# Kernel optimization log

Hardware: AMD Instinct MI355X
Metric: run time of the kernel (lower is better)

Reference implementation:

```python
import jax, jax.numpy as jnp
import numpy as np

N_NODES = 50000
N_EDGES = 1600000
F_IN = 128
C = 64          # block in/out channels
EF = 64         # edge MLP hidden dim
BLOCKS = 3
MLP_DIM = 128
N_CLASSES = 10
N_GRAPHS = 512
EPS = 1e-5


def setup_inputs() -> dict:
    key = jax.random.key(0)
    ks = jax.random.split(key, 32)
    s = 0.05
    inp = {
        "x": jax.random.normal(ks[0], (N_NODES, F_IN), jnp.float32),
        "edge_index": jax.random.randint(ks[1], (2, N_EDGES), 0, N_NODES, jnp.int64),
        "batch": jnp.sort(jax.random.randint(ks[2], (N_NODES,), 0, N_GRAPHS, jnp.int64)),
        "fc0_w": jax.random.normal(ks[3], (F_IN, C), jnp.float32) * s,
        "fc0_b": jnp.zeros((C,), jnp.float32),
        "fc1_w": jax.random.normal(ks[4], (BLOCKS * C, MLP_DIM), jnp.float32) * s,
        "fc1_b": jnp.zeros((MLP_DIM,), jnp.float32),
        "fc2_w": jax.random.normal(ks[5], (MLP_DIM, N_CLASSES), jnp.float32) * s,
        "fc2_b": jnp.zeros((N_CLASSES,), jnp.float32),
    }
    for i in range(BLOCKS):
        k = 6 + 4 * i
        inp[f"bn_g{i}"] = jnp.ones((C,), jnp.float32)
        inp[f"bn_b{i}"] = jnp.zeros((C,), jnp.float32)
        inp[f"w1_{i}"] = jax.random.normal(ks[k], (2 * C, EF), jnp.float32) * s
        inp[f"b1_{i}"] = jnp.zeros((EF,), jnp.float32)
        inp[f"w2_{i}"] = jax.random.normal(ks[k + 1], (EF, C), jnp.float32) * s
        inp[f"b2_{i}"] = jnp.zeros((C,), jnp.float32)
    return inp


def _batchnorm(x, g, b):
    mu = jnp.mean(x, axis=0)
    var = jnp.var(x, axis=0)
    return (x - mu) * jax.lax.rsqrt(var + EPS) * g + b


def _edge_conv(x, src, dst, w1, b1, w2, b2):
    # PyG-style EdgeConv: msg = MLP(concat[x_i, x_j - x_i]), max-aggregate at i
    xi = x[dst]                                  # [E, C]
    xj = x[src]                                  # [E, C]
    h = jax.nn.relu(jnp.concatenate([xi, xj - xi], axis=-1) @ w1 + b1)  # [E, EF]
    m = h @ w2 + b2                              # [E, C]
    agg = jax.ops.segment_max(m, dst, num_segments=N_NODES)
    return jnp.where(jnp.isfinite(agg), agg, 0.0)


def reference(x, edge_index, batch, fc0_w, fc0_b, fc1_w, fc1_b, fc2_w, fc2_b,
              bn_g0, bn_b0, w1_0, b1_0, w2_0, b2_0,
              bn_g1, bn_b1, w1_1, b1_1, w2_1, b2_1,
              bn_g2, bn_b2, w1_2, b1_2, w2_2, b2_2):
    src, dst = edge_index[0], edge_index[1]
    h = x @ fc0_w + fc0_b                        # [N, C]
    blocks = [(bn_g0, bn_b0, w1_0, b1_0, w2_0, b2_0),
              (bn_g1, bn_b1, w1_1, b1_1, w2_1, b2_1),
              (bn_g2, bn_b2, w1_2, b1_2, w2_2, b2_2)]
    xs = []
    for (g, b, w1, b1, w2, b2) in blocks:
        h = _batchnorm(h, g, b)
        h = jax.nn.relu(_edge_conv(h, src, dst, w1, b1, w2, b2))
        xs.append(h)
    cat = jnp.concatenate(xs, axis=-1)           # [N, 3C]
    # global mean pool over graphs
    sums = jax.ops.segment_sum(cat, batch, num_segments=N_GRAPHS)
    cnt = jax.ops.segment_sum(jnp.ones((N_NODES,), cat.dtype), batch,
                              num_segments=N_GRAPHS)
    pooled = sums / jnp.maximum(cnt, 1.0)[:, None]   # [G, 3C]
    hid = jax.nn.relu(pooled @ fc1_w + fc1_b)
    return jax.nn.log_softmax(hid @ fc2_w + fc2_b, axis=-1)
```

## Files before the change

kernel.cpp:

```cpp
#include <hip/hip_runtime.h>
#include <math.h>

#define N_NODES 50000
#define N_TILES 3125
#define N_EDGES 1600000
#define F_IN 128
#define C 64
#define EF 64
#define N_GRAPHS 512
#define MLP_DIM 128
#define N_CLASSES 10
#define EPS 1e-5f
#define NB 196
#define CAPB 16384
#define CHUNK 4096
#define NSLICE 8

typedef __attribute__((ext_vector_type(8))) _Float16 half8;
typedef __attribute__((ext_vector_type(2))) _Float16 half2v;
typedef __attribute__((ext_vector_type(4))) float floatx4;
typedef __attribute__((ext_vector_type(4))) unsigned uintx4;

union Uh { uintx4 v; half2v h[4]; half8 h8; };

__device__ __forceinline__ unsigned short f2h(float a) {
    union { _Float16 f; unsigned short u; } c;
    c.f = (_Float16)a;
    return c.u;
}
__device__ __forceinline__ float h2f(unsigned short u) {
    union { unsigned short u; _Float16 f; } c;
    c.u = u;
    return (float)c.f;
}
__device__ __forceinline__ half2v pk2(float a, float b) {
    auto t = __builtin_amdgcn_cvt_pkrtz(a, b);
    union { decltype(t) i; half2v o; } c;
    c.i = t;
    return c.o;
}

__global__ __launch_bounds__(256) void pass1_kernel(const int* __restrict__ src,
                                                    const int* __restrict__ dst,
                                                    int* __restrict__ gcur,
                                                    unsigned* __restrict__ keys) {
    __shared__ int lcnt[NB], lbase[NB], lcnt2[NB];
    int tid = threadIdx.x;
    int e0 = blockIdx.x * CHUNK;
    unsigned k[CHUNK / 256];
    int bk[CHUNK / 256];
    for (int i = tid; i < NB; i += 256) lcnt[i] = 0;
    __syncthreads();
#pragma unroll
    for (int i = 0; i < CHUNK / 256; i++) {
        int e = e0 + i * 256 + tid;
        if (e < N_EDGES) {
            int d = dst[e];
            k[i] = ((unsigned)d << 16) | (unsigned)src[e];
            bk[i] = d >> 8;
            atomicAdd(&lcnt[bk[i]], 1);
        } else bk[i] = -1;
    }
    __syncthreads();
    for (int i = tid; i < NB; i += 256) {
        int c = lcnt[i];
        lbase[i] = c ? atomicAdd(&gcur[i], c) : 0;
        lcnt2[i] = 0;
    }
    __syncthreads();
#pragma unroll
    for (int i = 0; i < CHUNK / 256; i++) {
        if (bk[i] >= 0) {
            int r = atomicAdd(&lcnt2[bk[i]], 1);
            keys[(size_t)bk[i] * CAPB + lbase[bk[i]] + r] = k[i];
        }
    }
}

__global__ __launch_bounds__(256) void node_count_kernel(const unsigned* __restrict__ keys,
                                                         const int* __restrict__ bcnt,
                                                         int* __restrict__ cnt) {
    __shared__ int lc[256];
    int tid = threadIdx.x;
    int b = blockIdx.x >> 1, half = blockIdx.x & 1;
    lc[tid] = 0;
    __syncthreads();
    int nk = bcnt[b];
    int chunk = (nk + 1) >> 1;
    int beg = half * chunk;
    int end = beg + chunk; if (end > nk) end = nk;
    const unsigned* kb = keys + (size_t)b * CAPB;
    for (int p = beg + tid; p < end; p += 256)
        atomicAdd(&lc[(kb[p] >> 16) & 255], 1);
    __syncthreads();
    int node = b * 256 + tid;
    if (node < N_NODES && lc[tid]) atomicAdd(&cnt[node], lc[tid]);
}

__global__ void pscan_kernel(const int* __restrict__ cnt, int* __restrict__ bbase,
                             int* __restrict__ row_start) {
    __shared__ int a[256];
    int tid = threadIdx.x;
    int sum = 0;
    if (tid < NB) {
        int base = tid * 256;
        for (int i = 0; i < 256; i++) {
            int node = base + i;
            if (node < N_NODES) sum += (cnt[node] + 15) & ~15;
        }
    }
    a[tid] = sum;
    __syncthreads();
    for (int off = 1; off < 256; off <<= 1) {
        int t = (tid >= off) ? a[tid - off] : 0;
        __syncthreads();
        a[tid] += t;
        __syncthreads();
    }
    int excl = a[tid] - sum;
    if (tid < NB) bbase[tid] = excl;
    if (tid == NB - 1) row_start[N_NODES] = excl + sum;
}

__global__ __launch_bounds__(256) void pass2_kernel(const unsigned* __restrict__ keys,
                                                    const int* __restrict__ bcnt,
                                                    const int* __restrict__ cnt,
                                                    const int* __restrict__ bbase,
                                                    int* __restrict__ row_start,
                                                    unsigned short* __restrict__ sorted_src) {
    __shared__ int loc[256], rs[256], cur[256];
    int tid = threadIdx.x, b = blockIdx.x;
    int node = b * 256 + tid;
    int c = (node < N_NODES) ? cnt[node] : 0;
    int pc = (c + 15) & ~15;
    loc[tid] = pc;
    cur[tid] = 0;
    __syncthreads();
    for (int off = 1; off < 256; off <<= 1) {
        int t = (tid >= off) ? loc[tid - off] : 0;
        __syncthreads();
        loc[tid] += t;
        __syncthreads();
    }
    int myrs = bbase[b] + loc[tid] - pc;
    rs[tid] = myrs;
    if (node < N_NODES) row_start[node] = myrs;
    __syncthreads();
    int beg = b * CAPB, end = beg + bcnt[b];
    for (int p = beg + tid; p < end; p += 256) {
        unsigned k = keys[p];
        int lidx = (k >> 16) & 255;
        int r = atomicAdd(&cur[lidx], 1);
        sorted_src[rs[lidx] + r] = (unsigned short)(k & 0xFFFFu);
    }
    __syncthreads();
    if (node < N_NODES) {
        int deg = cur[tid];
        if (deg > 0) {
            unsigned short s0 = sorted_src[myrs];
            for (int p = myrs + deg; p < myrs + pc; p++) sorted_src[p] = s0;
        }
    }
}

__global__ __launch_bounds__(256, 3) void fc0_mfma_kernel(const float* __restrict__ x,
                                                          const float* __restrict__ w,
                                                          const float* __restrict__ b,
                                                          unsigned short* __restrict__ h0,
                                                          float* __restrict__ bns) {
    __shared__ float bl1[4][64], bl2[4][64];
    int tid = threadIdx.x, lane = tid & 63, wid = tid >> 6;
    int q = lane >> 4, cl = lane & 15, kq = q * 8;

    Uh wf[4][4];
#pragma unroll
    for (int kh = 0; kh < 4; kh++)
#pragma unroll
        for (int cb = 0; cb < 4; cb++)
#pragma unroll
            for (int j = 0; j < 4; j++) {
                int k0 = kh * 32 + kq + 2 * j;
                int col = cb * 16 + cl;
                wf[kh][cb].h[j] = pk2(w[k0 * 64 + col], w[(k0 + 1) * 64 + col]);
            }
    float bv[4];
#pragma unroll
    for (int cb = 0; cb < 4; cb++) bv[cb] = b[cb * 16 + cl];
    float s1[4] = {0, 0, 0, 0}, s2[4] = {0, 0, 0, 0};

    for (int t = blockIdx.x * 4 + wid; t < N_TILES; t += gridDim.x * 4) {
        int nb = t * 16;
        floatx4 acc[4] = {{0,0,0,0},{0,0,0,0},{0,0,0,0},{0,0,0,0}};
#pragma unroll
        for (int kh = 0; kh < 4; kh++) {
            const float* xr = x + (size_t)(nb + cl) * F_IN + kh * 32 + kq;
            floatx4 xa = *(const floatx4*)xr;
            floatx4 xb = *(const floatx4*)(xr + 4);
            Uh xf;
            xf.h[0] = pk2(xa.x, xa.y); xf.h[1] = pk2(xa.z, xa.w);
            xf.h[2] = pk2(xb.x, xb.y); xf.h[3] = pk2(xb.z, xb.w);
#pragma unroll
            for (int cb = 0; cb < 4; cb++)
                acc[cb] = __builtin_amdgcn_mfma_f32_16x16x32_f16(xf.h8, wf[kh][cb].h8, acc[cb], 0, 0, 0);
        }
#pragma unroll
        for (int cb = 0; cb < 4; cb++)
#pragma unroll
            for (int r = 0; r < 4; r++) {
                float v = acc[cb][r] + bv[cb];
                h0[(size_t)(nb + q * 4 + r) * 64 + cb * 16 + cl] = f2h(v);
                s1[cb] += v; s2[cb] += v * v;
            }
    }
#pragma unroll
    for (int cb = 0; cb < 4; cb++) {
        s1[cb] += __shfl_xor(s1[cb], 16); s1[cb] += __shfl_xor(s1[cb], 32);
        s2[cb] += __shfl_xor(s2[cb], 16); s2[cb] += __shfl_xor(s2[cb], 32);
    }
    if (lane < 16) {
#pragma unroll
        for (int cb = 0; cb < 4; cb++) { bl1[wid][cb * 16 + lane] = s1[cb]; bl2[wid][cb * 16 + lane] = s2[cb]; }
    }
    __syncthreads();
    if (tid < 64) {
        float a  = bl1[0][tid] + bl1[1][tid] + bl1[2][tid] + bl1[3][tid];
        float c2 = bl2[0][tid] + bl2[1][tid] + bl2[2][tid] + bl2[3][tid];
        int sl = blockIdx.x & (NSLICE - 1);
        atomicAdd(&bns[sl * 128 + tid], a);
        atomicAdd(&bns[sl * 128 + 64 + tid], c2);
    }
}

__global__ __launch_bounds__(256, 4) void ab_mfma_kernel(const unsigned short* __restrict__ h,
                                                         const float* __restrict__ bns,
                                                         const float* __restrict__ g,
                                                         const float* __restrict__ bb,
                                                         const float* __restrict__ w1,
                                                         const float* __restrict__ b1,
                                                         unsigned short* __restrict__ A,
                                                         unsigned short* __restrict__ Bb) {
    __shared__ float scale[64], shift[64], cab[128];
    int tid = threadIdx.x, lane = tid & 63, wid = tid >> 6;
    int q = lane >> 4, cl = lane & 15, kq = q * 8;

    if (tid < 64) {
        float s1v = 0.f, s2v = 0.f;
#pragma unroll
        for (int s = 0; s < NSLICE; s++) { s1v += bns[s * 128 + tid]; s2v += bns[s * 128 + 64 + tid]; }
        float mu  = s1v * (1.0f / N_NODES);
        float var = s2v * (1.0f / N_NODES) - mu * mu;
        float sc  = g[tid] * rsqrtf(var + EPS);
        scale[tid] = sc;
        shift[tid] = bb[tid] - mu * sc;
    }
    __syncthreads();
    if (tid < 128) {
        int j = tid & 63;
        float acc = (tid < 64) ? b1[j] : 0.f;
        for (int k = 0; k < 64; k++) {
            float wa_ = w1[k * EF + j], wb_ = w1[(64 + k) * EF + j];
            acc = fmaf(shift[k], (tid < 64) ? (wa_ - wb_) : wb_, acc);
        }
        cab[tid] = acc;
    }
    Uh wa[2][4], wb[2][4];
#pragma unroll
    for (int kh = 0; kh < 2; kh++)
#pragma unroll
        for (int cb = 0; cb < 4; cb++)
#pragma unroll
            for (int j = 0; j < 4; j++) {
                int k0 = kh * 32 + kq + 2 * j;
                int col = cb * 16 + cl;
                float sa = scale[k0], sb = scale[k0 + 1];
                float a0 = w1[k0 * EF + col], b0 = w1[(64 + k0) * EF + col];
                float a1 = w1[(k0 + 1) * EF + col], b1v = w1[(64 + k0 + 1) * EF + col];
                wa[kh][cb].h[j] = pk2(sa * (a0 - b0), sb * (a1 - b1v));
                wb[kh][cb].h[j] = pk2(sa * b0, sb * b1v);
            }
    __syncthreads();
    float cav[4], cbv[4];
#pragma unroll
    for (int cb = 0; cb < 4; cb++) { cav[cb] = cab[cb * 16 + cl]; cbv[cb] = cab[64 + cb * 16 + cl]; }

    for (int t = blockIdx.x * 4 + wid; t < N_TILES; t += gridDim.x * 4) {
        int nb = t * 16;
        const unsigned short* hrow = h + (size_t)(nb + cl) * 64 + kq;
        Uh h0f, h1f;
        h0f.v = *(const uintx4*)hrow;
        h1f.v = *(const uintx4*)(hrow + 32);
        floatx4 accA[4] = {{0,0,0,0},{0,0,0,0},{0,0,0,0},{0,0,0,0}};
        floatx4 accB[4] = {{0,0,0,0},{0,0,0,0},{0,0,0,0},{0,0,0,0}};
#pragma unroll
        for (int cb = 0; cb < 4; cb++) {
            accA[cb] = __builtin_amdgcn_mfma_f32_16x16x32_f16(h0f.h8, wa[0][cb].h8, accA[cb], 0, 0, 0);
            accB[cb] = __builtin_amdgcn_mfma_f32_16x16x32_f16(h0f.h8, wb[0][cb].h8, accB[cb], 0, 0, 0);
            accA[cb] = __builtin_amdgcn_mfma_f32_16x16x32_f16(h1f.h8, wa[1][cb].h8, accA[cb], 0, 0, 0);
            accB[cb] = __builtin_amdgcn_mfma_f32_16x16x32_f16(h1f.h8, wb[1][cb].h8, accB[cb], 0, 0, 0);
        }
#pragma unroll
        for (int cb = 0; cb < 4; cb++)
#pragma unroll
            for (int r = 0; r < 4; r++) {
                size_t o = (size_t)(nb + q * 4 + r) * 64 + cb * 16 + cl;
                A[o]  = f2h(accA[cb][r] + cav[cb]);
                Bb[o] = f2h(accB[cb][r] + cbv[cb]);
            }
    }
}

__global__ __launch_bounds__(256, 4) void edge_mfma_kernel(
        const unsigned short* __restrict__ A, const unsigned short* __restrict__ Bb,
        const int* __restrict__ row_start, const unsigned short* __restrict__ sorted_src,
        const float* __restrict__ w2, const float* __restrict__ b2,
        unsigned short* __restrict__ catp, float* __restrict__ bnsNext) {
    __shared__ float r1[4][64], r2[4][64];
    int tid = threadIdx.x, lane = tid & 63, wid = tid >> 6;
    int kq = (lane >> 4) * 8;
    int cl = lane & 15;

    Uh bfr[2][4];
#pragma unroll
    for (int kh = 0; kh < 2; kh++)
#pragma unroll
        for (int cb = 0; cb < 4; cb++)
#pragma unroll
            for (int j = 0; j < 4; j++) {
                _Float16 w0 = (_Float16)w2[(kh * 32 + kq + 2 * j) * 64 + cb * 16 + cl];
                _Float16 w1 = (_Float16)w2[(kh * 32 + kq + 2 * j + 1) * 64 + cb * 16 + cl];
                bfr[kh][cb].h[j] = half2v{w0, w1};
            }
    float b2j = b2[lane];
    float s1 = 0.f, s2 = 0.f;
    const half2v zeroh = {(_Float16)0.f, (_Float16)0.f};

    for (int n = blockIdx.x * 4 + wid; n < N_NODES; n += gridDim.x * 4) {
        int beg = row_start[n], end = row_start[n + 1];
        const unsigned short* arow = A + (size_t)n * 64 + kq;
        Uh a0u, a1u;
        a0u.v = *(const uintx4*)(arow);
        a1u.v = *(const uintx4*)(arow + 32);
        floatx4 rmax0 = {-INFINITY, -INFINITY, -INFINITY, -INFINITY};
        floatx4 rmax1 = rmax0, rmax2 = rmax0, rmax3 = rmax0;

        auto tile = [&](uintx4 u0, uintx4 u1) {
            Uh b0u, b1u, f0, f1;
            b0u.v = u0; b1u.v = u1;
#pragma unroll
            for (int j = 0; j < 4; j++) {
                f0.h[j] = __builtin_elementwise_max(a0u.h[j] + b0u.h[j], zeroh);
                f1.h[j] = __builtin_elementwise_max(a1u.h[j] + b1u.h[j], zeroh);
            }
            floatx4 acc0 = {0.f, 0.f, 0.f, 0.f}, acc1 = acc0, acc2 = acc0, acc3 = acc0;
            acc0 = __builtin_amdgcn_mfma_f32_16x16x32_f16(f0.h8, bfr[0][0].h8, acc0, 0, 0, 0);
            acc1 = __builtin_amdgcn_mfma_f32_16x16x32_f16(f0.h8, bfr[0][1].h8, acc1, 0, 0, 0);
            acc2 = __builtin_amdgcn_mfma_f32_16x16x32_f16(f0.h8, bfr[0][2].h8, acc2, 0, 0, 0);
            acc3 = __builtin_amdgcn_mfma_f32_16x16x32_f16(f0.h8, bfr[0][3].h8, acc3, 0, 0, 0);
            acc0 = __builtin_amdgcn_mfma_f32_16x16x32_f16(f1.h8, bfr[1][0].h8, acc0, 0, 0, 0);
            acc1 = __builtin_amdgcn_mfma_f32_16x16x32_f16(f1.h8, bfr[1][1].h8, acc1, 0, 0, 0);
            acc2 = __builtin_amdgcn_mfma_f32_16x16x32_f16(f1.h8, bfr[1][2].h8, acc2, 0, 0, 0);
            acc3 = __builtin_amdgcn_mfma_f32_16x16x32_f16(f1.h8, bfr[1][3].h8, acc3, 0, 0, 0);
            rmax0 = __builtin_elementwise_max(rmax0, acc0);
            rmax1 = __builtin_elementwise_max(rmax1, acc1);
            rmax2 = __builtin_elementwise_max(rmax2, acc2);
            rmax3 = __builtin_elementwise_max(rmax3, acc3);
        };
        auto gather = [&](int p, uintx4& u0, uintx4& u1) {
            int srcm = sorted_src[p + cl];
            const unsigned short* brow = Bb + (size_t)srcm * 64 + kq;
            u0 = *(const uintx4*)(brow);
            u1 = *(const uintx4*)(brow + 32);
        };

        int p0 = beg;
        for (; p0 + 32 <= end; p0 += 32) {
            uintx4 x0, x1, y0, y1;
            gather(p0, x0, x1);
            gather(p0 + 16, y0, y1);
            tile(x0, x1);
            tile(y0, y1);
        }
        if (p0 < end) {
            uintx4 x0, x1;
            gather(p0, x0, x1);
            tile(x0, x1);
        }

        float v0 = fmaxf(fmaxf(rmax0.x, rmax0.y), fmaxf(rmax0.z, rmax0.w));
        float v1 = fmaxf(fmaxf(rmax1.x, rmax1.y), fmaxf(rmax1.z, rmax1.w));
        float v2 = fmaxf(fmaxf(rmax2.x, rmax2.y), fmaxf(rmax2.z, rmax2.w));
        float v3 = fmaxf(fmaxf(rmax3.x, rmax3.y), fmaxf(rmax3.z, rmax3.w));
        v0 = fmaxf(v0, __shfl_xor(v0, 16)); v0 = fmaxf(v0, __shfl_xor(v0, 32));
        v1 = fmaxf(v1, __shfl_xor(v1, 16)); v1 = fmaxf(v1, __shfl_xor(v1, 32));
        v2 = fmaxf(v2, __shfl_xor(v2, 16)); v2 = fmaxf(v2, __shfl_xor(v2, 32));
        v3 = fmaxf(v3, __shfl_xor(v3, 16)); v3 = fmaxf(v3, __shfl_xor(v3, 32));
        float vs = (lane & 32) ? ((lane & 16) ? v3 : v2) : ((lane & 16) ? v1 : v0);
        float v = fmaxf(vs + b2j, 0.f);
        catp[(size_t)n * 64 + lane] = f2h(v);
        s1 += v; s2 += v * v;
    }

    if (bnsNext) {
        r1[wid][lane] = s1; r2[wid][lane] = s2;
        __syncthreads();
        if (tid < 64) {
            float a  = r1[0][tid] + r1[1][tid] + r1[2][tid] + r1[3][tid];
            float c2 = r2[0][tid] + r2[1][tid] + r2[2][tid] + r2[3][tid];
            int sl = blockIdx.x & (NSLICE - 1);
            atomicAdd(&bnsNext[sl * 128 + tid], a);
            atomicAdd(&bnsNext[sl * 128 + 64 + tid], c2);
        }
    }
}

__global__ __launch_bounds__(192) void poolhead_kernel(const unsigned short* __restrict__ cat0,
                                                       const unsigned short* __restrict__ cat1,
                                                       const unsigned short* __restrict__ cat2,
                                                       const int* __restrict__ batch,
                                                       const float* __restrict__ fc1w,
                                                       const float* __restrict__ fc1b,
                                                       const float* __restrict__ fc2w,
                                                       const float* __restrict__ fc2b,
                                                       float* __restrict__ out) {
    __shared__ int se[2];
    __shared__ float p[192];
    __shared__ float hid[128];
    __shared__ float z[10];
    __shared__ float lse;
    int g = blockIdx.x, tid = threadIdx.x;
    if (tid < 2) {
        int target = g + tid;
        int lo = 0, hi = N_NODES;
        while (lo < hi) { int mid = (lo + hi) >> 1; if (batch[mid] < target) lo = mid + 1; else hi = mid; }
        se[tid] = lo;
    }
    __syncthreads();
    int s = se[0], e = se[1];
    const unsigned short* plane = (tid < 64) ? cat0 : ((tid < 128) ? cat1 : cat2);
    int col = tid & 63;
    float a0 = 0.f, a1 = 0.f, a2 = 0.f, a3 = 0.f;
    int r = s;
    for (; r + 4 <= e; r += 4) {
        a0 += h2f(plane[(size_t)(r + 0) * 64 + col]);
        a1 += h2f(plane[(size_t)(r + 1) * 64 + col]);
        a2 += h2f(plane[(size_t)(r + 2) * 64 + col]);
        a3 += h2f(plane[(size_t)(r + 3) * 64 + col]);
    }
    for (; r < e; r++) a0 += h2f(plane[(size_t)r * 64 + col]);
    float acc = (a0 + a1) + (a2 + a3);
    float denom = (e > s) ? (float)(e - s) : 1.0f;
    p[tid] = acc / denom;
    __syncthreads();
    if (tid < MLP_DIM) {
        float a = fc1b[tid];
        for (int k = 0; k < 192; k++) a = fmaf(p[k], fc1w[k * 128 + tid], a);
        hid[tid] = fmaxf(a, 0.f);
    }
    __syncthreads();
    if (tid < N_CLASSES) {
        float a = fc2b[tid];
        for (int k = 0; k < 128; k++) a = fmaf(hid[k], fc2w[k * 10 + tid], a);
        z[tid] = a;
    }
    __syncthreads();
    if (tid == 0) {
        float m = z[0];
        for (int i = 1; i < 10; i++) m = fmaxf(m, z[i]);
        float sm = 0.f;
        for (int i = 0; i < 10; i++) sm += expf(z[i] - m);
        lse = m + logf(sm);
    }
    __syncthreads();
    if (tid < N_CLASSES) out[g * 10 + tid] = z[tid] - lse;
}

extern "C" void kernel_launch(void* const* d_in, const int* in_sizes, int n_in,
                              void* d_out, int out_size, void* d_ws, size_t ws_size,
                              hipStream_t stream) {
    (void)in_sizes; (void)n_in; (void)out_size; (void)ws_size;
    const float* x    = (const float*)d_in[0];
    const int*   ei   = (const int*)d_in[1];
    const int*   batch= (const int*)d_in[2];
    const float* fc0w = (const float*)d_in[3];
    const float* fc0b = (const float*)d_in[4];
    const float* fc1w = (const float*)d_in[5];
    const float* fc1b = (const float*)d_in[6];
    const float* fc2w = (const float*)d_in[7];
    const float* fc2b = (const float*)d_in[8];
    const int* src = ei;
    const int* dst = ei + N_EDGES;
    float* out = (float*)d_out;

    char* w = (char*)d_ws;
    size_t off = 0;
    auto alloc = [&](size_t bytes) -> void* {
        void* p = w + off;
        off = (off + bytes + 255) & ~(size_t)255;
        return p;
    };
    const size_t MAX_PAD_EDGES = (size_t)N_EDGES + 16 * (size_t)N_NODES;

    const size_t BNS_OFF = 1024;
    const size_t CNT_OFF = BNS_OFF + 3 * NSLICE * 128 * 4;
    const size_t ZBYTES  = CNT_OFF + (size_t)N_NODES * 4;
    char* zbase = (char*)alloc(ZBYTES);
    int*   gcur   = (int*)zbase;
    float* bnsAll = (float*)(zbase + BNS_OFF);
    int*   cnt    = (int*)(zbase + CNT_OFF);

    unsigned short* cat0 = (unsigned short*)alloc((size_t)N_NODES * 64 * 2);
    unsigned short* cat1 = (unsigned short*)alloc((size_t)N_NODES * 64 * 2);
    unsigned short* cat2 = (unsigned short*)alloc((size_t)N_NODES * 64 * 2);
    unsigned short* h0   = (unsigned short*)alloc((size_t)N_NODES * 64 * 2);
    unsigned short* Ae   = (unsigned short*)alloc((size_t)N_NODES * 64 * 2);
    unsigned short* Be   = (unsigned short*)alloc((size_t)N_NODES * 64 * 2);
    unsigned* keys = (unsigned*)alloc((size_t)NB * CAPB * 4);
    unsigned short* sorted_src = (unsigned short*)alloc(MAX_PAD_EDGES * 2);
    int*   row_start = (int*)alloc((size_t)(N_NODES + 1) * 4);
    int*   bbase   = (int*)alloc(NB * 4);

    (void)hipMemsetAsync(zbase, 0, ZBYTES, stream);

    pass1_kernel<<<(N_EDGES + CHUNK - 1) / CHUNK, 256, 0, stream>>>(src, dst, gcur, keys);
    node_count_kernel<<<NB * 2, 256, 0, stream>>>(keys, gcur, cnt);
    pscan_kernel<<<1, 256, 0, stream>>>(cnt, bbase, row_start);
    pass2_kernel<<<NB, 256, 0, stream>>>(keys, gcur, cnt, bbase, row_start, sorted_src);

    fc0_mfma_kernel<<<782, 256, 0, stream>>>(x, fc0w, fc0b, h0, bnsAll);

    unsigned short* planes[3] = {cat0, cat1, cat2};
    for (int blk = 0; blk < 3; blk++) {
        const float* g  = (const float*)d_in[9 + 6 * blk];
        const float* bb = (const float*)d_in[10 + 6 * blk];
        const float* w1 = (const float*)d_in[11 + 6 * blk];
        const float* b1 = (const float*)d_in[12 + 6 * blk];
        const float* w2 = (const float*)d_in[13 + 6 * blk];
        const float* b2 = (const float*)d_in[14 + 6 * blk];
        const unsigned short* hsrc = (blk == 0) ? h0 : planes[blk - 1];

        ab_mfma_kernel<<<782, 256, 0, stream>>>(hsrc, bnsAll + blk * NSLICE * 128,
                                                g, bb, w1, b1, Ae, Be);
        edge_mfma_kernel<<<2048, 256, 0, stream>>>(
            Ae, Be, row_start, sorted_src, w2, b2, planes[blk],
            (blk < 2) ? (bnsAll + (blk + 1) * NSLICE * 128) : nullptr);
    }

    poolhead_kernel<<<N_GRAPHS, 192, 0, stream>>>(cat0, cat1, cat2, batch,
                                                  fc1w, fc1b, fc2w, fc2b, out);
}
```

Measured before the change: 428.6 us.

## Fuse graph-sort preprocessing kernels with fc0 and first AB projection launches

The edge bucketing pass now runs in the same launch as the fc0 projection, and the per-node degree count shares a launch with the first block's AB projection, using disjoint block ranges. The single-block prefix-scan kernel is removed. pass2 now claims each bucket's output base with an atomic on a global counter, and the edge kernel computes a row's end from its own count. This cuts the number of launches and the serialized small kernels, at the cost of a non-monotonic CSR layout and larger fused kernels sharing launch bounds.

```diff
diff --git a/kernel.cpp b/kernel.cpp
--- a/kernel.cpp
+++ b/kernel.cpp
@@ -14,6 +14,8 @@
 #define NB 196
 #define CAPB 16384
 #define CHUNK 4096
+#define NPASS1 391
+#define NFC0 782
 #define NSLICE 8
 
 typedef __attribute__((ext_vector_type(8))) _Float16 half8;
@@ -40,136 +42,51 @@
     return c.o;
 }
 
-__global__ __launch_bounds__(256) void pass1_kernel(const int* __restrict__ src,
-                                                    const int* __restrict__ dst,
-                                                    int* __restrict__ gcur,
-                                                    unsigned* __restrict__ keys) {
+__global__ __launch_bounds__(256, 3) void fc0_pass1_kernel(
+        const int* __restrict__ src, const int* __restrict__ dst,
+        int* __restrict__ gcur, unsigned* __restrict__ keys,
+        const float* __restrict__ x, const float* __restrict__ w,
+        const float* __restrict__ b, unsigned short* __restrict__ h0,
+        float* __restrict__ bns) {
     __shared__ int lcnt[NB], lbase[NB], lcnt2[NB];
+    __shared__ float bl1[4][64], bl2[4][64];
     int tid = threadIdx.x;
-    int e0 = blockIdx.x * CHUNK;
-    unsigned k[CHUNK / 256];
-    int bk[CHUNK / 256];
-    for (int i = tid; i < NB; i += 256) lcnt[i] = 0;
-    __syncthreads();
-#pragma unroll
-    for (int i = 0; i < CHUNK / 256; i++) {
-        int e = e0 + i * 256 + tid;
-        if (e < N_EDGES) {
-            int d = dst[e];
-            k[i] = ((unsigned)d << 16) | (unsigned)src[e];
-            bk[i] = d >> 8;
-            atomicAdd(&lcnt[bk[i]], 1);
-        } else bk[i] = -1;
-    }
-    __syncthreads();
-    for (int i = tid; i < NB; i += 256) {
-        int c = lcnt[i];
-        lbase[i] = c ? atomicAdd(&gcur[i], c) : 0;
-        lcnt2[i] = 0;
-    }
-    __syncthreads();
-#pragma unroll
-    for (int i = 0; i < CHUNK / 256; i++) {
-        if (bk[i] >= 0) {
-            int r = atomicAdd(&lcnt2[bk[i]], 1);
-            keys[(size_t)bk[i] * CAPB + lbase[bk[i]] + r] = k[i];
-        }
-    }
-}
-
-__global__ __launch_bounds__(256) void node_count_kernel(const unsigned* __restrict__ keys,
-                                                         const int* __restrict__ bcnt,
-                                                         int* __restrict__ cnt) {
-    __shared__ int lc[256];
-    int tid = threadIdx.x;
-    int b = blockIdx.x >> 1, half = blockIdx.x & 1;
-    lc[tid] = 0;
-    __syncthreads();
-    int nk = bcnt[b];
-    int chunk = (nk + 1) >> 1;
-    int beg = half * chunk;
-    int end = beg + chunk; if (end > nk) end = nk;
-    const unsigned* kb = keys + (size_t)b * CAPB;
-    for (int p = beg + tid; p < end; p += 256)
-        atomicAdd(&lc[(kb[p] >> 16) & 255], 1);
-    __syncthreads();
-    int node = b * 256 + tid;
-    if (node < N_NODES && lc[tid]) atomicAdd(&cnt[node], lc[tid]);
-}
-
-__global__ void pscan_kernel(const int* __restrict__ cnt, int* __restrict__ bbase,
-                             int* __restrict__ row_start) {
-    __shared__ int a[256];
-    int tid = threadIdx.x;
-    int sum = 0;
-    if (tid < NB) {
-        int base = tid * 256;
-        for (int i = 0; i < 256; i++) {
-            int node = base + i;
-            if (node < N_NODES) sum += (cnt[node] + 15) & ~15;
-        }
-    }
-    a[tid] = sum;
-    __syncthreads();
-    for (int off = 1; off < 256; off <<= 1) {
-        int t = (tid >= off) ? a[tid - off] : 0;
-        __syncthreads();
-        a[tid] += t;
-        __syncthreads();
-    }
-    int excl = a[tid] - sum;
-    if (tid < NB) bbase[tid] = excl;
-    if (tid == NB - 1) row_start[N_NODES] = excl + sum;
-}
-
-__global__ __launch_bounds__(256) void pass2_kernel(const unsigned* __restrict__ keys,
-                                                    const int* __restrict__ bcnt,
-                                                    const int* __restrict__ cnt,
-                                                    const int* __restrict__ bbase,
-                                                    int* __restrict__ row_start,
-                                                    unsigned short* __restrict__ sorted_src) {
-    __shared__ int loc[256], rs[256], cur[256];
-    int tid = threadIdx.x, b = blockIdx.x;
-    int node = b * 256 + tid;
-    int c = (node < N_NODES) ? cnt[node] : 0;
-    int pc = (c + 15) & ~15;
-    loc[tid] = pc;
-    cur[tid] = 0;
-    __syncthreads();
-    for (int off = 1; off < 256; off <<= 1) {
-        int t = (tid >= off) ? loc[tid - off] : 0;
-        __syncthreads();
-        loc[tid] += t;
-        __syncthreads();
-    }
-    int myrs = bbase[b] + loc[tid] - pc;
-    rs[tid] = myrs;
-    if (node < N_NODES) row_start[node] = myrs;
-    __syncthreads();
-    int beg = b * CAPB, end = beg + bcnt[b];
-    for (int p = beg + tid; p < end; p += 256) {
-        unsigned k = keys[p];
-        int lidx = (k >> 16) & 255;
-        int r = atomicAdd(&cur[lidx], 1);
-        sorted_src[rs[lidx] + r] = (unsigned short)(k & 0xFFFFu);
-    }
-    __syncthreads();
-    if (node < N_NODES) {
-        int deg = cur[tid];
-        if (deg > 0) {
-            unsigned short s0 = sorted_src[myrs];
-            for (int p = myrs + deg; p < myrs + pc; p++) sorted_src[p] = s0;
-        }
-    }
-}
-
-__global__ __launch_bounds__(256, 3) void fc0_mfma_kernel(const float* __restrict__ x,
-                                                          const float* __restrict__ w,
-                                                          const float* __restrict__ b,
-                                                          unsigned short* __restrict__ h0,
-                                                          float* __restrict__ bns) {
-    __shared__ float bl1[4][64], bl2[4][64];
-    int tid = threadIdx.x, lane = tid & 63, wid = tid >> 6;
+
+    if (blockIdx.x < NPASS1) {
+        int e0 = blockIdx.x * CHUNK;
+        unsigned k[CHUNK / 256];
+        int bk[CHUNK / 256];
+        for (int i = tid; i < NB; i += 256) lcnt[i] = 0;
+        __syncthreads();
+#pragma unroll
+        for (int i = 0; i < CHUNK / 256; i++) {
+            int e = e0 + i * 256 + tid;
+            if (e < N_EDGES) {
+                int d = dst[e];
+                k[i] = ((unsigned)d << 16) | (unsigned)src[e];
+                bk[i] = d >> 8;
+                atomicAdd(&lcnt[bk[i]], 1);
+            } else bk[i] = -1;
+        }
+        __syncthreads();
+        for (int i = tid; i < NB; i += 256) {
+            int c = lcnt[i];
+            lbase[i] = c ? atomicAdd(&gcur[i], c) : 0;
+            lcnt2[i] = 0;
+        }
+        __syncthreads();
+#pragma unroll
+        for (int i = 0; i < CHUNK / 256; i++) {
+            if (bk[i] >= 0) {
+                int r = atomicAdd(&lcnt2[bk[i]], 1);
+                keys[(size_t)bk[i] * CAPB + lbase[bk[i]] + r] = k[i];
+            }
+        }
+        return;
+    }
+
+    int bid = blockIdx.x - NPASS1;
+    int lane = tid & 63, wid = tid >> 6;
     int q = lane >> 4, cl = lane & 15, kq = q * 8;
 
     Uh wf[4][4];
@@ -188,7 +105,7 @@
     for (int cb = 0; cb < 4; cb++) bv[cb] = b[cb * 16 + cl];
     float s1[4] = {0, 0, 0, 0}, s2[4] = {0, 0, 0, 0};
 
-    for (int t = blockIdx.x * 4 + wid; t < N_TILES; t += gridDim.x * 4) {
+    for (int t = bid * 4 + wid; t < N_TILES; t += NFC0 * 4) {
         int nb = t * 16;
         floatx4 acc[4] = {{0,0,0,0},{0,0,0,0},{0,0,0,0},{0,0,0,0}};
 #pragma unroll
@@ -225,22 +142,23 @@
     if (tid < 64) {
         float a  = bl1[0][tid] + bl1[1][tid] + bl1[2][tid] + bl1[3][tid];
         float c2 = bl2[0][tid] + bl2[1][tid] + bl2[2][tid] + bl2[3][tid];
-        int sl = blockIdx.x & (NSLICE - 1);
+        int sl = bid & (NSLICE - 1);
         atomicAdd(&bns[sl * 128 + tid], a);
         atomicAdd(&bns[sl * 128 + 64 + tid], c2);
     }
 }
 
-__global__ __launch_bounds__(256, 4) void ab_mfma_kernel(const unsigned short* __restrict__ h,
-                                                         const float* __restrict__ bns,
-                                                         const float* __restrict__ g,
-                                                         const float* __restrict__ bb,
-                                                         const float* __restrict__ w1,
-                                                         const float* __restrict__ b1,
-                                                         unsigned short* __restrict__ A,
-                                                         unsigned short* __restrict__ Bb) {
-    __shared__ float scale[64], shift[64], cab[128];
-    int tid = threadIdx.x, lane = tid & 63, wid = tid >> 6;
+__device__ __forceinline__ void ab_body(int bid, int tid,
+                                        const unsigned short* __restrict__ h,
+                                        const float* __restrict__ bns,
+                                        const float* __restrict__ g,
+                                        const float* __restrict__ bb,
+                                        const float* __restrict__ w1,
+                                        const float* __restrict__ b1,
+                                        unsigned short* __restrict__ A,
+                                        unsigned short* __restrict__ Bb,
+                                        float* scale, float* shift, float* cab) {
+    int lane = tid & 63, wid = tid >> 6;
     int q = lane >> 4, cl = lane & 15, kq = q * 8;
 
     if (tid < 64) {
@@ -283,7 +201,7 @@
 #pragma unroll
     for (int cb = 0; cb < 4; cb++) { cav[cb] = cab[cb * 16 + cl]; cbv[cb] = cab[64 + cb * 16 + cl]; }
 
-    for (int t = blockIdx.x * 4 + wid; t < N_TILES; t += gridDim.x * 4) {
+    for (int t = bid * 4 + wid; t < N_TILES; t += NFC0 * 4) {
         int nb = t * 16;
         const unsigned short* hrow = h + (size_t)(nb + cl) * 64 + kq;
         Uh h0f, h1f;
@@ -309,9 +227,92 @@
     }
 }
 
+__global__ __launch_bounds__(256, 4) void nc_ab_kernel(
+        const unsigned* __restrict__ keys, const int* __restrict__ bcnt,
+        int* __restrict__ cnt,
+        const unsigned short* __restrict__ h, const float* __restrict__ bns,
+        const float* __restrict__ g, const float* __restrict__ bb,
+        const float* __restrict__ w1, const float* __restrict__ b1,
+        unsigned short* __restrict__ A, unsigned short* __restrict__ Bb) {
+    __shared__ int lc[256];
+    __shared__ float scale[64], shift[64], cab[128];
+    int tid = threadIdx.x;
+    if (blockIdx.x < 2 * NB) {
+        int b = blockIdx.x >> 1, half = blockIdx.x & 1;
+        lc[tid] = 0;
+        __syncthreads();
+        int nk = bcnt[b];
+        int chunk = (nk + 1) >> 1;
+        int beg = half * chunk;
+        int end = beg + chunk; if (end > nk) end = nk;
+        const unsigned* kb = keys + (size_t)b * CAPB;
+        for (int p = beg + tid; p < end; p += 256)
+            atomicAdd(&lc[(kb[p] >> 16) & 255], 1);
+        __syncthreads();
+        int node = b * 256 + tid;
+        if (node < N_NODES && lc[tid]) atomicAdd(&cnt[node], lc[tid]);
+        return;
+    }
+    ab_body(blockIdx.x - 2 * NB, tid, h, bns, g, bb, w1, b1, A, Bb, scale, shift, cab);
+}
+
+__global__ __launch_bounds__(256, 4) void ab_mfma_kernel(
+        const unsigned short* __restrict__ h, const float* __restrict__ bns,
+        const float* __restrict__ g, const float* __restrict__ bb,
+        const float* __restrict__ w1, const float* __restrict__ b1,
+        unsigned short* __restrict__ A, unsigned short* __restrict__ Bb) {
+    __shared__ float scale[64], shift[64], cab[128];
+    ab_body(blockIdx.x, threadIdx.x, h, bns, g, bb, w1, b1, A, Bb, scale, shift, cab);
+}
+
+__global__ __launch_bounds__(256) void pass2_kernel(const unsigned* __restrict__ keys,
+                                                    const int* __restrict__ bcnt,
+                                                    const int* __restrict__ cnt,
+                                                    int* __restrict__ gtotal,
+                                                    int* __restrict__ row_start,
+                                                    unsigned short* __restrict__ sorted_src) {
+    __shared__ int loc[256], rs[256], cur[256];
+    __shared__ int base;
+    int tid = threadIdx.x, b = blockIdx.x;
+    int node = b * 256 + tid;
+    int c = (node < N_NODES) ? cnt[node] : 0;
+    int pc = (c + 15) & ~15;
+    loc[tid] = pc;
+    cur[tid] = 0;
+    __syncthreads();
+    for (int off = 1; off < 256; off <<= 1) {
+        int t = (tid >= off) ? loc[tid - off] : 0;
+        __syncthreads();
+        loc[tid] += t;
+        __syncthreads();
+    }
+    if (tid == 255) base = atomicAdd(gtotal, loc[255]);
+    __syncthreads();
+    int myrs = base + loc[tid] - pc;
+    rs[tid] = myrs;
+    if (node < N_NODES) row_start[node] = myrs;
+    __syncthreads();
+    int beg = b * CAPB, end = beg + bcnt[b];
+    for (int p = beg + tid; p < end; p += 256) {
+        unsigned k = keys[p];
+        int lidx = (k >> 16) & 255;
+        int r = atomicAdd(&cur[lidx], 1);
+        sorted_src[rs[lidx] + r] = (unsigned short)(k & 0xFFFFu);
+    }
+    __syncthreads();
+    if (node < N_NODES) {
+        int deg = cur[tid];
+        if (deg > 0) {
+            unsigned short s0 = sorted_src[myrs];
+            for (int p = myrs + deg; p < myrs + pc; p++) sorted_src[p] = s0;
+        }
+    }
+}
+
 __global__ __launch_bounds__(256, 4) void edge_mfma_kernel(
         const unsigned short* __restrict__ A, const unsigned short* __restrict__ Bb,
-        const int* __restrict__ row_start, const unsigned short* __restrict__ sorted_src,
+        const int* __restrict__ row_start, const int* __restrict__ cnt,
+        const unsigned short* __restrict__ sorted_src,
         const float* __restrict__ w2, const float* __restrict__ b2,
         unsigned short* __restrict__ catp, float* __restrict__ bnsNext) {
     __shared__ float r1[4][64], r2[4][64];
@@ -335,7 +336,8 @@
     const half2v zeroh = {(_Float16)0.f, (_Float16)0.f};
 
     for (int n = blockIdx.x * 4 + wid; n < N_NODES; n += gridDim.x * 4) {
-        int beg = row_start[n], end = row_start[n + 1];
+        int beg = row_start[n];
+        int end = beg + ((cnt[n] + 15) & ~15);
         const unsigned short* arow = A + (size_t)n * 64 + kq;
         Uh a0u, a1u;
         a0u.v = *(const uintx4*)(arow);
@@ -500,11 +502,12 @@
     };
     const size_t MAX_PAD_EDGES = (size_t)N_EDGES + 16 * (size_t)N_NODES;
 
-    const size_t BNS_OFF = 1024;
+    const size_t BNS_OFF = 1280;
     const size_t CNT_OFF = BNS_OFF + 3 * NSLICE * 128 * 4;
     const size_t ZBYTES  = CNT_OFF + (size_t)N_NODES * 4;
     char* zbase = (char*)alloc(ZBYTES);
     int*   gcur   = (int*)zbase;
+    int*   gtotal = (int*)(zbase + 1024);
     float* bnsAll = (float*)(zbase + BNS_OFF);
     int*   cnt    = (int*)(zbase + CNT_OFF);
 
@@ -516,32 +519,30 @@
     unsigned short* Be   = (unsigned short*)alloc((size_t)N_NODES * 64 * 2);
     unsigned* keys = (unsigned*)alloc((size_t)NB * CAPB * 4);
     unsigned short* sorted_src = (unsigned short*)alloc(MAX_PAD_EDGES * 2);
-    int*   row_start = (int*)alloc((size_t)(N_NODES + 1) * 4);
-    int*   bbase   = (int*)alloc(NB * 4);
+    int*   row_start = (int*)alloc((size_t)N_NODES * 4);
 
     (void)hipMemsetAsync(zbase, 0, ZBYTES, stream);
 
-    pass1_kernel<<<(N_EDGES + CHUNK - 1) / CHUNK, 256, 0, stream>>>(src, dst, gcur, keys);
-    node_count_kernel<<<NB * 2, 256, 0, stream>>>(keys, gcur, cnt);
-    pscan_kernel<<<1, 256, 0, stream>>>(cnt, bbase, row_start);
-    pass2_kernel<<<NB, 256, 0, stream>>>(keys, gcur, cnt, bbase, row_start, sorted_src);
-
-    fc0_mfma_kernel<<<782, 256, 0, stream>>>(x, fc0w, fc0b, h0, bnsAll);
+    fc0_pass1_kernel<<<NPASS1 + NFC0, 256, 0, stream>>>(src, dst, gcur, keys,
+                                                        x, fc0w, fc0b, h0, bnsAll);
+    nc_ab_kernel<<<2 * NB + NFC0, 256, 0, stream>>>(
+        keys, gcur, cnt, h0, bnsAll,
+        (const float*)d_in[9], (const float*)d_in[10],
+        (const float*)d_in[11], (const float*)d_in[12], Ae, Be);
+    pass2_kernel<<<NB, 256, 0, stream>>>(keys, gcur, cnt, gtotal, row_start, sorted_src);
 
     unsigned short* planes[3] = {cat0, cat1, cat2};
     for (int blk = 0; blk < 3; blk++) {
-        const float* g  = (const float*)d_in[9 + 6 * blk];
-        const float* bb = (const float*)d_in[10 + 6 * blk];
-        const float* w1 = (const float*)d_in[11 + 6 * blk];
-        const float* b1 = (const float*)d_in[12 + 6 * blk];
         const float* w2 = (const float*)d_in[13 + 6 * blk];
         const float* b2 = (const float*)d_in[14 + 6 * blk];
-        const unsigned short* hsrc = (blk == 0) ? h0 : planes[blk - 1];
-
-        ab_mfma_kernel<<<782, 256, 0, stream>>>(hsrc, bnsAll + blk * NSLICE * 128,
-                                                g, bb, w1, b1, Ae, Be);
+        if (blk > 0) {
+            ab_mfma_kernel<<<NFC0, 256, 0, stream>>>(
+                planes[blk - 1], bnsAll + blk * NSLICE * 128,
+                (const float*)d_in[9 + 6 * blk], (const float*)d_in[10 + 6 * blk],
+                (const float*)d_in[11 + 6 * blk], (const float*)d_in[12 + 6 * blk], Ae, Be);
+        }
         edge_mfma_kernel<<<2048, 256, 0, stream>>>(
-            Ae, Be, row_start, sorted_src, w2, b2, planes[blk],
+            Ae, Be, row_start, cnt, sorted_src, w2, b2, planes[blk],
             (blk < 2) ? (bnsAll + (blk + 1) * NSLICE * 128) : nullptr);
     }
 
```

Measured after the change: 397.4 us. 1.08x faster.
